# Kernel tuning notes

Hardware: AMD Instinct MI355X
Metric: run time of the kernel (lower is better)

## Reference

```python
import jax, jax.numpy as jnp
import numpy as np

N_NODES = 50000
N_EDGES = 800000
N_LABEL_EDGES = 200000
IN_CH = 256
HID = 64
OUT_CH = 64


def gcn_conv(x, W, b, edge_index, n_nodes):
    """PyG GCNConv: symmetric-normalized aggregation with self-loops.
    out[col] = sum_row norm(row,col) * (x @ W)[row] + b
    """
    xw = x @ W  # [N, out]
    loops = jnp.arange(n_nodes, dtype=edge_index.dtype)
    row = jnp.concatenate([edge_index[0], loops])  # source
    col = jnp.concatenate([edge_index[1], loops])  # target
    deg = jax.ops.segment_sum(jnp.ones_like(col, dtype=xw.dtype), col, num_segments=n_nodes)
    dis = jnp.where(deg > 0, jax.lax.rsqrt(deg), 0.0)
    norm = dis[row] * dis[col]  # [E+N]
    out = jax.ops.segment_sum(xw[row] * norm[:, None], col, num_segments=n_nodes)
    return out + b


def setup_inputs() -> dict:
    key = jax.random.key(0)
    k0, k1, k2, k3, k4 = jax.random.split(key, 5)
    x = jax.random.normal(k0, (N_NODES, IN_CH), dtype=jnp.float32)
    edge_index = jax.random.randint(k1, (2, N_EDGES), 0, N_NODES, dtype=jnp.int32)
    edge_label_index = jax.random.randint(k2, (2, N_LABEL_EDGES), 0, N_NODES, dtype=jnp.int32)
    W1 = jax.random.normal(k3, (IN_CH, HID), dtype=jnp.float32) * (1.0 / np.sqrt(IN_CH))
    b1 = jnp.zeros((HID,), dtype=jnp.float32)
    W2 = jax.random.normal(k4, (HID, OUT_CH), dtype=jnp.float32) * (1.0 / np.sqrt(HID))
    b2 = jnp.zeros((OUT_CH,), dtype=jnp.float32)
    return {"x": x, "edge_index": edge_index, "edge_label_index": edge_label_index,
            "W1": W1, "b1": b1, "W2": W2, "b2": b2}


def reference(x, edge_index, edge_label_index, W1, b1, W2, b2):
    n = x.shape[0]
    # encode: two GCNConv layers with ReLU between
    h = jax.nn.relu(gcn_conv(x, W1, b1, edge_index, n))
    z = gcn_conv(h, W2, b2, edge_index, n)
    # decode: gather node pairs, elementwise multiply, sum over features
    src, dst = edge_label_index[0], edge_label_index[1]
    return jnp.sum(z[src] * z[dst], axis=1)  # [N_LABEL_EDGES]
```

## Files before the change

kernel.cpp:

```cpp
#include <hip/hip_runtime.h>
#include <hip/hip_bf16.h>


constexpr int NC = 512;
constexpr int NBPAD = 256;
constexpr int BSHIFT = 8;

__device__ __forceinline__ unsigned short f2bf(float f) {
    unsigned u = __float_as_uint(f);
    return (unsigned short)((u + 0x7FFF + ((u >> 16) & 1)) >> 16);
}
__device__ __forceinline__ float bf2f(unsigned short h) {
    return __uint_as_float(((unsigned)h) << 16);
}
__device__ __forceinline__ float4 bf4_to_f4(ushort4 u) {
    return make_float4(bf2f(u.x), bf2f(u.y), bf2f(u.z), bf2f(u.w));
}

__global__ __launch_bounds__(256) void hist_kernel(const int* __restrict__ col,
                                                   int* __restrict__ histCM,
                                                   int* __restrict__ bsums, int E, int CE) {
    __shared__ int hl[NBPAD];
    const int t = threadIdx.x, c = blockIdx.x;
    hl[t] = 0;
    __syncthreads();
    const int s = c * CE, e = min(E, s + CE);
    for (int i = s + t; i < e; i += 256) atomicAdd(&hl[col[i] >> BSHIFT], 1);
    __syncthreads();
    const int v = hl[t];
    histCM[c * NBPAD + t] = v;
    if (v) atomicAdd(&bsums[t], v);
}

__global__ __launch_bounds__(256) void rowscan_kernel(const int* __restrict__ histCM,
                                                      const int* __restrict__ bsums,
                                                      int* __restrict__ offsBM) {
    __shared__ int red[256];
    __shared__ int sc[256];
    const int t = threadIdx.x, b = blockIdx.x;
    red[t] = (t < b) ? bsums[t] : 0;
    __syncthreads();
    for (int off = 128; off > 0; off >>= 1) {
        if (t < off) red[t] += red[t + off];
        __syncthreads();
    }
    const int base = red[0];
    const int a0 = histCM[(2 * t) * NBPAD + b];
    const int a1 = histCM[(2 * t + 1) * NBPAD + b];
    const int ps = a0 + a1;
    sc[t] = ps;
    __syncthreads();
    for (int off = 1; off < 256; off <<= 1) {
        int u = (t >= off) ? sc[t - off] : 0;
        __syncthreads();
        sc[t] += u;
        __syncthreads();
    }
    const int excl = sc[t] - ps;
    offsBM[b * NC + 2 * t] = base + excl;
    offsBM[b * NC + 2 * t + 1] = base + excl + a0;
}

__global__ __launch_bounds__(256) void reorder_kernel(const int* __restrict__ row,
                                                      const int* __restrict__ col,
                                                      const int* __restrict__ offsBM,
                                                      int* __restrict__ part, int E, int CE) {
    __shared__ int cur[NBPAD];
    const int t = threadIdx.x, c = blockIdx.x;
    cur[t] = offsBM[t * NC + c];
    __syncthreads();
    const int s = c * CE, e = min(E, s + CE);
    for (int i = s + t; i < e; i += 256) {
        const int r = row[i], cl = col[i];
        const int p = atomicAdd(&cur[cl >> BSHIFT], 1);
        part[p] = (r << 8) | (cl & 255);
    }
}

__global__ __launch_bounds__(256) void bucket_csr_kernel(const int* __restrict__ part,
                                                         const int* __restrict__ offsBM,
                                                         int* __restrict__ csr,
                                                         int* __restrict__ offs,
                                                         float* __restrict__ dis,
                                                         int N, int E, int nbk) {
    __shared__ int cnt[256];
    __shared__ int sc[256];
    const int t = threadIdx.x, b = blockIdx.x;
    const int base = b << BSHIFT;
    const int bstart = offsBM[b * NC];
    const int bend = (b + 1 < NBPAD) ? offsBM[(b + 1) * NC] : E;
    const int m = bend - bstart;
    cnt[t] = 0;
    __syncthreads();
    for (int i = t; i < m; i += 256) atomicAdd(&cnt[part[bstart + i] & 255], 1);
    __syncthreads();
    const int v = cnt[t];
    sc[t] = v;
    __syncthreads();
    for (int off = 1; off < 256; off <<= 1) {
        int u = (t >= off) ? sc[t - off] : 0;
        __syncthreads();
        sc[t] += u;
        __syncthreads();
    }
    const int excl = sc[t] - v;
    const int node = base + t;
    if (node < N) {
        offs[node] = bstart + excl;
        dis[node] = rsqrtf((float)(v + 1));
    }
    sc[t] = excl;
    __syncthreads();
    for (int i = t; i < m; i += 256) {
        const int pc = part[bstart + i];
        const int p = atomicAdd(&sc[pc & 255], 1);
        csr[bstart + p] = pc >> 8;
    }
    if (b == nbk - 1 && t == 0) offs[N] = E;
}

template <int K>
__global__ __launch_bounds__(256) void gemm_tile(const float* __restrict__ X,
                                                 const float* __restrict__ W,
                                                 const float* __restrict__ rowscale,
                                                 unsigned short* __restrict__ Y, int nrows) {
    __shared__ float sX[64 * 64];
    __shared__ float sW[64 * 64];
    const int tid = threadIdx.x;
    const int tx = tid & 15;
    const int ty = tid >> 4;
    const int rowbase = blockIdx.x * 64;

    float acc[16];
    #pragma unroll
    for (int i = 0; i < 16; ++i) acc[i] = 0.f;

    const int lr = tid & 63;
    const int lq = tid >> 6;
    int grow = rowbase + lr;
    if (grow >= nrows) grow = nrows - 1;
    const float* xrow = X + (long)grow * K;

    for (int kc = 0; kc < K; kc += 64) {
        if (kc) __syncthreads();
        #pragma unroll
        for (int i = 0; i < 4; ++i) {
            const int o = tid * 4 + i * 1024;
            *(float4*)&sW[o] = *(const float4*)&W[(long)kc * 64 + o];
        }
        #pragma unroll
        for (int t = 0; t < 4; ++t) {
            const int k = lq * 16 + t * 4;
            const float4 v = *(const float4*)&xrow[kc + k];
            sX[(k + 0) * 64 + lr] = v.x;
            sX[(k + 1) * 64 + lr] = v.y;
            sX[(k + 2) * 64 + lr] = v.z;
            sX[(k + 3) * 64 + lr] = v.w;
        }
        __syncthreads();
        #pragma unroll 4
        for (int k = 0; k < 64; ++k) {
            const float4 xv = *(const float4*)&sX[k * 64 + ty * 4];
            const float4 wv = *(const float4*)&sW[k * 64 + tx * 4];
            acc[0]  = fmaf(xv.x, wv.x, acc[0]);
            acc[1]  = fmaf(xv.x, wv.y, acc[1]);
            acc[2]  = fmaf(xv.x, wv.z, acc[2]);
            acc[3]  = fmaf(xv.x, wv.w, acc[3]);
            acc[4]  = fmaf(xv.y, wv.x, acc[4]);
            acc[5]  = fmaf(xv.y, wv.y, acc[5]);
            acc[6]  = fmaf(xv.y, wv.z, acc[6]);
            acc[7]  = fmaf(xv.y, wv.w, acc[7]);
            acc[8]  = fmaf(xv.z, wv.x, acc[8]);
            acc[9]  = fmaf(xv.z, wv.y, acc[9]);
            acc[10] = fmaf(xv.z, wv.z, acc[10]);
            acc[11] = fmaf(xv.z, wv.w, acc[11]);
            acc[12] = fmaf(xv.w, wv.x, acc[12]);
            acc[13] = fmaf(xv.w, wv.y, acc[13]);
            acc[14] = fmaf(xv.w, wv.z, acc[14]);
            acc[15] = fmaf(xv.w, wv.w, acc[15]);
        }
    }

    #pragma unroll
    for (int i = 0; i < 4; ++i) {
        const int orow = rowbase + ty * 4 + i;
        if (orow < nrows) {
            const float d = rowscale[orow];
            ushort4 ov;
            ov.x = f2bf(d * acc[i * 4 + 0]);
            ov.y = f2bf(d * acc[i * 4 + 1]);
            ov.z = f2bf(d * acc[i * 4 + 2]);
            ov.w = f2bf(d * acc[i * 4 + 3]);
            *(ushort4*)&Y[(long)orow * 64 + tx * 4] = ov;
        }
    }
}

template <bool RELU, bool OUT_BF16>
__global__ __launch_bounds__(256) void agg_kernel(const unsigned short* __restrict__ xs,
                                                  const int* __restrict__ csr,
                                                  const int* __restrict__ offs,
                                                  const float* __restrict__ dis,
                                                  const float* __restrict__ bias,
                                                  void* __restrict__ out, int n) {
    const int t = threadIdx.x;
    const int fl = t & 15;
    const int i = blockIdx.x * 16 + (t >> 4);
    if (i >= n) return;
    float4 acc = bf4_to_f4(*(const ushort4*)&xs[(long)i * 64 + fl * 4]);
    const int s = offs[i];
    const int e = offs[i + 1];
    int j = s;
    for (; j + 3 < e; j += 4) {
        const int r0 = csr[j],     r1 = csr[j + 1];
        const int r2 = csr[j + 2], r3 = csr[j + 3];
        const float4 v0 = bf4_to_f4(*(const ushort4*)&xs[(long)r0 * 64 + fl * 4]);
        const float4 v1 = bf4_to_f4(*(const ushort4*)&xs[(long)r1 * 64 + fl * 4]);
        const float4 v2 = bf4_to_f4(*(const ushort4*)&xs[(long)r2 * 64 + fl * 4]);
        const float4 v3 = bf4_to_f4(*(const ushort4*)&xs[(long)r3 * 64 + fl * 4]);
        acc.x += (v0.x + v1.x) + (v2.x + v3.x);
        acc.y += (v0.y + v1.y) + (v2.y + v3.y);
        acc.z += (v0.z + v1.z) + (v2.z + v3.z);
        acc.w += (v0.w + v1.w) + (v2.w + v3.w);
    }
    for (; j < e; ++j) {
        const int r0 = csr[j];
        const float4 v0 = bf4_to_f4(*(const ushort4*)&xs[(long)r0 * 64 + fl * 4]);
        acc.x += v0.x; acc.y += v0.y; acc.z += v0.z; acc.w += v0.w;
    }
    const float di = dis[i];
    const float4 b = *(const float4*)&bias[fl * 4];
    float4 o;
    o.x = fmaf(acc.x, di, b.x); o.y = fmaf(acc.y, di, b.y);
    o.z = fmaf(acc.z, di, b.z); o.w = fmaf(acc.w, di, b.w);
    if (RELU) {
        o.x = fmaxf(o.x, 0.f); o.y = fmaxf(o.y, 0.f);
        o.z = fmaxf(o.z, 0.f); o.w = fmaxf(o.w, 0.f);
    }
    if (OUT_BF16) {
        ushort4 ov;
        ov.x = f2bf(o.x); ov.y = f2bf(o.y); ov.z = f2bf(o.z); ov.w = f2bf(o.w);
        *(ushort4*)&((unsigned short*)out)[(long)i * 64 + fl * 4] = ov;
    } else {
        *(float4*)&((float*)out)[(long)i * 64 + fl * 4] = o;
    }
}

__global__ __launch_bounds__(256) void decode_kernel(const unsigned short* __restrict__ z,
                                                     const int* __restrict__ src,
                                                     const int* __restrict__ dst,
                                                     float* __restrict__ out, int L) {
    const int t = blockIdx.x * 256 + threadIdx.x;
    const int e = t >> 4;
    const int fl = t & 15;
    if (e >= L) return;
    const int s = src[e];
    const int d = dst[e];
    const float4 a = bf4_to_f4(*(const ushort4*)&z[(long)s * 64 + fl * 4]);
    const float4 b = bf4_to_f4(*(const ushort4*)&z[(long)d * 64 + fl * 4]);
    float p = a.x * b.x + a.y * b.y + a.z * b.z + a.w * b.w;
    p += __shfl_xor(p, 8); p += __shfl_xor(p, 4);
    p += __shfl_xor(p, 2); p += __shfl_xor(p, 1);
    if (fl == 0) out[e] = p;
}

extern "C" void kernel_launch(void* const* d_in, const int* in_sizes, int n_in,
                              void* d_out, int out_size, void* d_ws, size_t ws_size,
                              hipStream_t stream) {
    const float* x   = (const float*)d_in[0];
    const int*   ei  = (const int*)d_in[1];
    const int*   eli = (const int*)d_in[2];
    const float* W1  = (const float*)d_in[3];
    const float* b1  = (const float*)d_in[4];
    const float* W2  = (const float*)d_in[5];
    const float* b2  = (const float*)d_in[6];
    float* out = (float*)d_out;

    const int N = in_sizes[0] / 256;
    const int E = in_sizes[1] / 2;
    const int L = in_sizes[2] / 2;
    const int* row = ei;
    const int* col = ei + E;
    const int* src = eli;
    const int* dst = eli + L;

    char* w = (char*)d_ws;
    unsigned short* xs = (unsigned short*)w;  w += (size_t)N * 64 * 2;
    float* h   = (float*)w;  w += (size_t)N * 64 * 4;
    unsigned short* z = (unsigned short*)w;  w += (size_t)N * 64 * 2;
    int*   csr = (int*)w;    w += (size_t)E * 4;
    int*   offs = (int*)w;   w += (size_t)(N + 1) * 4;
    float* dis = (float*)w;  w += (size_t)N * 4;
    int*   part = (int*)w;   w += (size_t)E * 4;
    int* histCM = (int*)w;   w += (size_t)NC * NBPAD * 4;
    int* offsBM = (int*)w;   w += (size_t)NBPAD * NC * 4;
    int* bsums  = (int*)w;   w += NBPAD * 4;

    const int CE = (E + NC - 1) / NC;
    const int nbk = (N + (1 << BSHIFT) - 1) >> BSHIFT;

    hipMemsetAsync(bsums, 0, NBPAD * sizeof(int), stream);
    hist_kernel<<<NC, 256, 0, stream>>>(col, histCM, bsums, E, CE);
    rowscan_kernel<<<NBPAD, 256, 0, stream>>>(histCM, bsums, offsBM);
    reorder_kernel<<<NC, 256, 0, stream>>>(row, col, offsBM, part, E, CE);
    bucket_csr_kernel<<<nbk, 256, 0, stream>>>(part, offsBM, csr, offs, dis, N, E, nbk);

    gemm_tile<256><<<(N + 63) / 64, 256, 0, stream>>>(x, W1, dis, xs, N);
    agg_kernel<true, false><<<(N + 15) / 16, 256, 0, stream>>>(xs, csr, offs, dis, b1, h, N);
    gemm_tile<64><<<(N + 63) / 64, 256, 0, stream>>>(h, W2, dis, xs, N);
    agg_kernel<false, true><<<(N + 15) / 16, 256, 0, stream>>>(xs, csr, offs, dis, b2, z, N);
    decode_kernel<<<(L + 15) / 16, 256, 0, stream>>>(z, src, dst, out, L);
}
```

Before: 224.9 us.

## Use bf16 MFMA for first-layer GEMM and prefetch CSR indices in aggregation

Replaces the first-layer FP32 tiled shared-memory GEMM (K=256) with a wave-level bf16 MFMA kernel. The weights are pre-packed into a bf16 fragment-friendly layout by a small new kernel, and X rows are converted to bf16 on the fly. The aggregation loop also software-prefetches the next four CSR neighbor indices to overlap index loads with feature gathers. This adds an extra launch and bf16 rounding of the inputs to the first GEMM.

After: 216.1 us. 1.04x faster.

```diff
diff --git a/kernel.cpp b/kernel.cpp
--- a/kernel.cpp
+++ b/kernel.cpp
@@ -5,6 +5,9 @@
 constexpr int NC = 512;
 constexpr int NBPAD = 256;
 constexpr int BSHIFT = 8;
+
+using short8 = __attribute__((ext_vector_type(8))) short;
+using f32x4 = __attribute__((ext_vector_type(4))) float;
 
 __device__ __forceinline__ unsigned short f2bf(float f) {
     unsigned u = __float_as_uint(f);
@@ -117,6 +120,68 @@
         csr[bstart + p] = pc >> 8;
     }
     if (b == nbk - 1 && t == 0) offs[N] = E;
+}
+
+__global__ __launch_bounds__(256) void pack_w_kernel(const float* __restrict__ W,
+                                                     unsigned short* __restrict__ Wp, int K) {
+    const int k = threadIdx.x;
+    if (k < K) {
+        for (int c = 0; c < 64; ++c)
+            Wp[((k >> 3) * 64 + c) * 8 + (k & 7)] = f2bf(W[k * 64 + c]);
+    }
+}
+
+template <int K>
+__global__ __launch_bounds__(256) void gemm_mfma(const float* __restrict__ X,
+                                                 const unsigned short* __restrict__ Wp,
+                                                 const float* __restrict__ rowscale,
+                                                 unsigned short* __restrict__ Y, int nrows) {
+    const int tid = threadIdx.x;
+    const int wv = tid >> 6;
+    const int lane = tid & 63;
+    const int m = lane & 15;
+    const int quad = lane >> 4;
+    const int rowbase = blockIdx.x * 64 + wv * 16;
+
+    int grow = rowbase + m;
+    if (grow >= nrows) grow = nrows - 1;
+    const float* xrow = X + (long)grow * K + quad * 8;
+
+    f32x4 acc0 = {0.f, 0.f, 0.f, 0.f};
+    f32x4 acc1 = acc0, acc2 = acc0, acc3 = acc0;
+
+    #pragma unroll
+    for (int ks = 0; ks < K / 32; ++ks) {
+        const float4 a0 = *(const float4*)(xrow + ks * 32);
+        const float4 a1 = *(const float4*)(xrow + ks * 32 + 4);
+        short8 af;
+        af[0] = (short)f2bf(a0.x); af[1] = (short)f2bf(a0.y);
+        af[2] = (short)f2bf(a0.z); af[3] = (short)f2bf(a0.w);
+        af[4] = (short)f2bf(a1.x); af[5] = (short)f2bf(a1.y);
+        af[6] = (short)f2bf(a1.z); af[7] = (short)f2bf(a1.w);
+        const unsigned short* bp = Wp + (size_t)((ks * 4 + quad) * 64) * 8;
+        const short8 b0 = *(const short8*)(bp + (0 * 16 + m) * 8);
+        const short8 b1 = *(const short8*)(bp + (1 * 16 + m) * 8);
+        const short8 b2 = *(const short8*)(bp + (2 * 16 + m) * 8);
+        const short8 b3 = *(const short8*)(bp + (3 * 16 + m) * 8);
+        acc0 = __builtin_amdgcn_mfma_f32_16x16x32_bf16(af, b0, acc0, 0, 0, 0);
+        acc1 = __builtin_amdgcn_mfma_f32_16x16x32_bf16(af, b1, acc1, 0, 0, 0);
+        acc2 = __builtin_amdgcn_mfma_f32_16x16x32_bf16(af, b2, acc2, 0, 0, 0);
+        acc3 = __builtin_amdgcn_mfma_f32_16x16x32_bf16(af, b3, acc3, 0, 0, 0);
+    }
+
+    #pragma unroll
+    for (int reg = 0; reg < 4; ++reg) {
+        const int orow = rowbase + quad * 4 + reg;
+        if (orow < nrows) {
+            const float d = rowscale[orow];
+            unsigned short* yp = Y + (size_t)orow * 64 + m;
+            yp[0]  = f2bf(d * acc0[reg]);
+            yp[16] = f2bf(d * acc1[reg]);
+            yp[32] = f2bf(d * acc2[reg]);
+            yp[48] = f2bf(d * acc3[reg]);
+        }
+    }
 }
 
 template <int K>
@@ -211,9 +276,13 @@
     const int s = offs[i];
     const int e = offs[i + 1];
     int j = s;
-    for (; j + 3 < e; j += 4) {
-        const int r0 = csr[j],     r1 = csr[j + 1];
-        const int r2 = csr[j + 2], r3 = csr[j + 3];
+    int r0 = 0, r1 = 0, r2 = 0, r3 = 0;
+    if (j + 3 < e) { r0 = csr[j]; r1 = csr[j + 1]; r2 = csr[j + 2]; r3 = csr[j + 3]; }
+    while (j + 3 < e) {
+        const int jn = j + 4;
+        const int c0 = min(jn,     e - 1), c1 = min(jn + 1, e - 1);
+        const int c2 = min(jn + 2, e - 1), c3 = min(jn + 3, e - 1);
+        const int n0 = csr[c0], n1 = csr[c1], n2 = csr[c2], n3 = csr[c3];
         const float4 v0 = bf4_to_f4(*(const ushort4*)&xs[(long)r0 * 64 + fl * 4]);
         const float4 v1 = bf4_to_f4(*(const ushort4*)&xs[(long)r1 * 64 + fl * 4]);
         const float4 v2 = bf4_to_f4(*(const ushort4*)&xs[(long)r2 * 64 + fl * 4]);
@@ -222,11 +291,13 @@
         acc.y += (v0.y + v1.y) + (v2.y + v3.y);
         acc.z += (v0.z + v1.z) + (v2.z + v3.z);
         acc.w += (v0.w + v1.w) + (v2.w + v3.w);
+        r0 = n0; r1 = n1; r2 = n2; r3 = n3;
+        j = jn;
     }
     for (; j < e; ++j) {
-        const int r0 = csr[j];
-        const float4 v0 = bf4_to_f4(*(const ushort4*)&xs[(long)r0 * 64 + fl * 4]);
-        acc.x += v0.x; acc.y += v0.y; acc.z += v0.z; acc.w += v0.w;
+        const int r = csr[j];
+        const float4 v = bf4_to_f4(*(const ushort4*)&xs[(long)r * 64 + fl * 4]);
+        acc.x += v.x; acc.y += v.y; acc.z += v.z; acc.w += v.w;
     }
     const float di = dis[i];
     const float4 b = *(const float4*)&bias[fl * 4];
@@ -295,17 +366,19 @@
     int* histCM = (int*)w;   w += (size_t)NC * NBPAD * 4;
     int* offsBM = (int*)w;   w += (size_t)NBPAD * NC * 4;
     int* bsums  = (int*)w;   w += NBPAD * 4;
+    unsigned short* Wp1 = (unsigned short*)w;  w += (size_t)256 * 64 * 2;
 
     const int CE = (E + NC - 1) / NC;
     const int nbk = (N + (1 << BSHIFT) - 1) >> BSHIFT;
 
     hipMemsetAsync(bsums, 0, NBPAD * sizeof(int), stream);
+    pack_w_kernel<<<1, 256, 0, stream>>>(W1, Wp1, 256);
     hist_kernel<<<NC, 256, 0, stream>>>(col, histCM, bsums, E, CE);
     rowscan_kernel<<<NBPAD, 256, 0, stream>>>(histCM, bsums, offsBM);
     reorder_kernel<<<NC, 256, 0, stream>>>(row, col, offsBM, part, E, CE);
     bucket_csr_kernel<<<nbk, 256, 0, stream>>>(part, offsBM, csr, offs, dis, N, E, nbk);
 
-    gemm_tile<256><<<(N + 63) / 64, 256, 0, stream>>>(x, W1, dis, xs, N);
+    gemm_mfma<256><<<(N + 63) / 64, 256, 0, stream>>>(x, Wp1, dis, xs, N);
     agg_kernel<true, false><<<(N + 15) / 16, 256, 0, stream>>>(xs, csr, offs, dis, b1, h, N);
     gemm_tile<64><<<(N + 63) / 64, 256, 0, stream>>>(h, W2, dis, xs, N);
     agg_kernel<false, true><<<(N + 15) / 16, 256, 0, stream>>>(xs, csr, offs, dis, b2, z, N);
```
